# Kernel tuning notes

Hardware: AMD Instinct MI355X
Metric: run time of the kernel (lower is better)

The kernel has to match this reference:

```python
import jax, jax.numpy as jnp
import numpy as np

IMG_SIZES = [56, 28, 14, 7]


def setup_inputs() -> dict:
    key = jax.random.key(0)
    k0, k1, k2, k3, kp = jax.random.split(key, 5)
    return {
        "feat0": jax.random.normal(k0, (8, 64, 56, 56), dtype=jnp.float32),
        "feat1": jax.random.normal(k1, (8, 128, 28, 28), dtype=jnp.float32),
        "feat2": jax.random.normal(k2, (8, 256, 14, 14), dtype=jnp.float32),
        "feat3": jax.random.normal(k3, (8, 512, 7, 7), dtype=jnp.float32),
        "pts": jax.random.normal(kp, (131072, 3), dtype=jnp.float32),
        "batch": 3,
    }


def _project(feat, h, w, size):
    # feat: [C, size, size]; h, w: [N] float in [0, 223]
    x = h / (224.0 / size)
    y = w / (224.0 / size)
    x1 = jnp.floor(x).astype(jnp.int32)
    x2 = jnp.minimum(jnp.ceil(x).astype(jnp.int32), size - 1)
    y1 = jnp.floor(y).astype(jnp.int32)
    y2 = jnp.minimum(jnp.ceil(y).astype(jnp.int32), size - 1)
    # NOTE: original casts x,y to long BEFORE computing weights (truncation),
    # so weights are integer 0/1 -- reproduced faithfully.
    xl = x.astype(jnp.int32)
    yl = y.astype(jnp.int32)
    g = lambda xi, yi: feat[:, xi, yi].T  # [N, C] gather
    w11 = ((x2 - xl) * (y2 - yl)).astype(feat.dtype)[:, None]
    w12 = ((x2 - xl) * (yl - y1)).astype(feat.dtype)[:, None]
    w21 = ((xl - x1) * (y2 - yl)).astype(feat.dtype)[:, None]
    w22 = ((xl - x1) * (yl - y1)).astype(feat.dtype)[:, None]
    return w11 * g(x1, y1) + w21 * g(x2, y1) + w12 * g(x1, y2) + w22 * g(x2, y2)


def reference(feat0, feat1, feat2, feat3, pts, batch):
    h = 248.0 * (pts[:, 1] / pts[:, 2]) + 111.5
    w = 248.0 * (pts[:, 0] / (-pts[:, 2])) + 111.5
    h = jnp.clip(h, 0.0, 223.0)
    w = jnp.clip(w, 0.0, 223.0)
    feats = [feat0[batch], feat1[batch], feat2[batch], feat3[batch]]
    outs = [_project(f, h, w, s) for f, s in zip(feats, IMG_SIZES)]
    return jnp.concatenate(outs, axis=1)  # [N, 960]
```

## Files before the change

### kernel.cpp

```cpp
#include <hip/hip_runtime.h>
#include <hip/hip_bf16.h>

#define NPTS 131072
#define FT_TOTAL 376320

typedef float f32x4 __attribute__((ext_vector_type(4)));

__global__ __launch_bounds__(256) void k_indices(
    const float* __restrict__ pts,
    int4* __restrict__ idx4)
{
    int n = blockIdx.x * 256 + threadIdx.x;
    if (n >= NPTS) return;
    float px = pts[3 * n + 0];
    float py = pts[3 * n + 1];
    float pz = pts[3 * n + 2];
    float qh = __fdiv_rn(py, pz);
    float qw = __fdiv_rn(px, -pz);
    float h = __fadd_rn(__fmul_rn(248.0f, qh), 111.5f);
    float w = __fadd_rn(__fmul_rn(248.0f, qw), 111.5f);
    h = fminf(fmaxf(h, 0.0f), 223.0f);
    w = fminf(fmaxf(w, 0.0f), 223.0f);

    const float scl[4] = {0.25f, 0.125f, 0.0625f, 0.03125f};
    const int   S[4]   = {56, 28, 14, 7};
    int r[4];
#pragma unroll
    for (int s = 0; s < 4; ++s) {
        float x = h * scl[s];
        float y = w * scl[s];
        int x1 = (int)floorf(x);
        int x2 = min((int)ceilf(x), S[s] - 1);
        int y1 = (int)floorf(y);
        int y2 = min((int)ceilf(y), S[s] - 1);
        int bit = (x2 - x1) * (y2 - y1);
        r[s] = bit ? (x1 * S[s] + y1) : -1;
    }
    idx4[n] = make_int4(r[0], r[1], r[2], r[3]);
}

__global__ __launch_bounds__(256) void k_transpose(
    const float* __restrict__ f0,
    const float* __restrict__ f1,
    const float* __restrict__ f2,
    const float* __restrict__ f3,
    const int* __restrict__ batch,
    float* __restrict__ ft)
{
    int d = blockIdx.x * 256 + threadIdx.x;
    if (d >= FT_TOTAL) return;
    int b = *batch;
    const float* src;
    int local, c, p, hw;
    if (d < 200704) {
        local = d;          c = local & 63;  p = local >> 6; hw = 3136;
        src = f0 + (size_t)b * 64 * 3136;
    } else if (d < 301056) {
        local = d - 200704; c = local & 127; p = local >> 7; hw = 784;
        src = f1 + (size_t)b * 128 * 784;
    } else if (d < 351232) {
        local = d - 301056; c = local & 255; p = local >> 8; hw = 196;
        src = f2 + (size_t)b * 256 * 196;
    } else {
        local = d - 351232; c = local & 511; p = local >> 9; hw = 49;
        src = f3 + (size_t)b * 512 * 49;
    }
    ft[d] = src[c * hw + p];
}

__global__ __launch_bounds__(256) void k_gather(
    const int* __restrict__ idx,
    const float* __restrict__ ft,
    float* __restrict__ out)
{
    int gid = blockIdx.x * 256 + threadIdx.x;
    int n = gid / 240;
    int j = gid - n * 240;

    int s, C, toff, cb;
    if (j < 16)       { s = 0; C = 64;  toff = 0;      cb = j * 4; }
    else if (j < 48)  { s = 1; C = 128; toff = 200704; cb = (j - 16) * 4; }
    else if (j < 112) { s = 2; C = 256; toff = 301056; cb = (j - 48) * 4; }
    else              { s = 3; C = 512; toff = 351232; cb = (j - 112) * 4; }

    int id = idx[n * 4 + s];
    f32x4 v = (f32x4)(0.0f);
    if (id >= 0) {
        v = *(const f32x4*)(ft + toff + id * C + cb);
    }
    f32x4* dst = (f32x4*)(out + (size_t)n * 960 + j * 4);
    __builtin_nontemporal_store(v, dst);
}

extern "C" void kernel_launch(void* const* d_in, const int* in_sizes, int n_in,
                              void* d_out, int out_size, void* d_ws, size_t ws_size,
                              hipStream_t stream) {
    const float* f0  = (const float*)d_in[0];
    const float* f1  = (const float*)d_in[1];
    const float* f2  = (const float*)d_in[2];
    const float* f3  = (const float*)d_in[3];
    const float* pts = (const float*)d_in[4];
    const int* batch = (const int*)d_in[5];

    int4* idx4 = (int4*)d_ws;
    float* ft = (float*)((char*)d_ws + (size_t)NPTS * 16);
    float* out = (float*)d_out;

    k_indices<<<NPTS / 256, 256, 0, stream>>>(pts, idx4);
    k_transpose<<<(FT_TOTAL + 255) / 256, 256, 0, stream>>>(f0, f1, f2, f3, batch, ft);
    k_gather<<<122880, 256, 0, stream>>>((const int*)idx4, ft, out);
}
```

Baseline: 485.2 us.

## Fuse index computation into gather kernel with one wavefront per point

Removes the separate index kernel and its workspace round-trip. The gather kernel now maps one 64-lane wavefront to each point, computes the four projection indices inline, and has each lane write up to four float4 chunks of the 960-wide output row. This saves a launch and the index buffer traffic, and drops the per-thread divide by 240. In exchange every lane recomputes the division and projection math, and the fourth iteration leaves most lanes idle.

```diff
diff --git a/kernel.cpp b/kernel.cpp
--- a/kernel.cpp
+++ b/kernel.cpp
@@ -5,39 +5,6 @@
 #define FT_TOTAL 376320
 
 typedef float f32x4 __attribute__((ext_vector_type(4)));
-
-__global__ __launch_bounds__(256) void k_indices(
-    const float* __restrict__ pts,
-    int4* __restrict__ idx4)
-{
-    int n = blockIdx.x * 256 + threadIdx.x;
-    if (n >= NPTS) return;
-    float px = pts[3 * n + 0];
-    float py = pts[3 * n + 1];
-    float pz = pts[3 * n + 2];
-    float qh = __fdiv_rn(py, pz);
-    float qw = __fdiv_rn(px, -pz);
-    float h = __fadd_rn(__fmul_rn(248.0f, qh), 111.5f);
-    float w = __fadd_rn(__fmul_rn(248.0f, qw), 111.5f);
-    h = fminf(fmaxf(h, 0.0f), 223.0f);
-    w = fminf(fmaxf(w, 0.0f), 223.0f);
-
-    const float scl[4] = {0.25f, 0.125f, 0.0625f, 0.03125f};
-    const int   S[4]   = {56, 28, 14, 7};
-    int r[4];
-#pragma unroll
-    for (int s = 0; s < 4; ++s) {
-        float x = h * scl[s];
-        float y = w * scl[s];
-        int x1 = (int)floorf(x);
-        int x2 = min((int)ceilf(x), S[s] - 1);
-        int y1 = (int)floorf(y);
-        int y2 = min((int)ceilf(y), S[s] - 1);
-        int bit = (x2 - x1) * (y2 - y1);
-        r[s] = bit ? (x1 * S[s] + y1) : -1;
-    }
-    idx4[n] = make_int4(r[0], r[1], r[2], r[3]);
-}
 
 __global__ __launch_bounds__(256) void k_transpose(
     const float* __restrict__ f0,
@@ -69,27 +36,57 @@
 }
 
 __global__ __launch_bounds__(256) void k_gather(
-    const int* __restrict__ idx,
+    const float* __restrict__ pts,
     const float* __restrict__ ft,
     float* __restrict__ out)
 {
-    int gid = blockIdx.x * 256 + threadIdx.x;
-    int n = gid / 240;
-    int j = gid - n * 240;
+    int n = (blockIdx.x * 256 + threadIdx.x) >> 6;
+    int lane = threadIdx.x & 63;
 
-    int s, C, toff, cb;
-    if (j < 16)       { s = 0; C = 64;  toff = 0;      cb = j * 4; }
-    else if (j < 48)  { s = 1; C = 128; toff = 200704; cb = (j - 16) * 4; }
-    else if (j < 112) { s = 2; C = 256; toff = 301056; cb = (j - 48) * 4; }
-    else              { s = 3; C = 512; toff = 351232; cb = (j - 112) * 4; }
+    float px = pts[3 * n + 0];
+    float py = pts[3 * n + 1];
+    float pz = pts[3 * n + 2];
+    float qh = __fdiv_rn(py, pz);
+    float qw = __fdiv_rn(px, -pz);
+    float h = __fadd_rn(__fmul_rn(248.0f, qh), 111.5f);
+    float w = __fadd_rn(__fmul_rn(248.0f, qw), 111.5f);
+    h = fminf(fmaxf(h, 0.0f), 223.0f);
+    w = fminf(fmaxf(w, 0.0f), 223.0f);
 
-    int id = idx[n * 4 + s];
-    f32x4 v = (f32x4)(0.0f);
-    if (id >= 0) {
-        v = *(const f32x4*)(ft + toff + id * C + cb);
+    const float scl[4] = {0.25f, 0.125f, 0.0625f, 0.03125f};
+    const int   S[4]   = {56, 28, 14, 7};
+    int r[4];
+#pragma unroll
+    for (int s = 0; s < 4; ++s) {
+        float x = h * scl[s];
+        float y = w * scl[s];
+        int x1 = (int)floorf(x);
+        int x2 = min((int)ceilf(x), S[s] - 1);
+        int y1 = (int)floorf(y);
+        int y2 = min((int)ceilf(y), S[s] - 1);
+        int bit = (x2 - x1) * (y2 - y1);
+        r[s] = bit ? (x1 * S[s] + y1) : -1;
     }
-    f32x4* dst = (f32x4*)(out + (size_t)n * 960 + j * 4);
-    __builtin_nontemporal_store(v, dst);
+
+    float* rowout = out + (size_t)n * 960;
+#pragma unroll
+    for (int k = 0; k < 4; ++k) {
+        int j = 64 * k + lane;
+        if (j < 240) {
+            int s = (j >= 16) + (j >= 48) + (j >= 112);
+            int C    = 64 << s;
+            int toff = (s == 0) ? 0 : (s == 1) ? 200704 : (s == 2) ? 301056 : 351232;
+            int jb   = (s == 0) ? 0 : (s == 1) ? 16     : (s == 2) ? 48     : 112;
+            int cb   = (j - jb) * 4;
+
+            int id = r[s];
+            f32x4 v = (f32x4)(0.0f);
+            if (id >= 0) {
+                v = *(const f32x4*)(ft + toff + id * C + cb);
+            }
+            __builtin_nontemporal_store(v, (f32x4*)(rowout + j * 4));
+        }
+    }
 }
 
 extern "C" void kernel_launch(void* const* d_in, const int* in_sizes, int n_in,
@@ -102,11 +99,9 @@
     const float* pts = (const float*)d_in[4];
     const int* batch = (const int*)d_in[5];
 
-    int4* idx4 = (int4*)d_ws;
-    float* ft = (float*)((char*)d_ws + (size_t)NPTS * 16);
+    float* ft = (float*)d_ws;
     float* out = (float*)d_out;
 
-    k_indices<<<NPTS / 256, 256, 0, stream>>>(pts, idx4);
     k_transpose<<<(FT_TOTAL + 255) / 256, 256, 0, stream>>>(f0, f1, f2, f3, batch, ft);
-    k_gather<<<122880, 256, 0, stream>>>((const int*)idx4, ft, out);
+    k_gather<<<NPTS / 4, 256, 0, stream>>>(pts, ft, out);
 }
```

Result: no change. 488.3 us (+0.6%).

## Stage coarse-scale feature tables in LDS and use persistent specialized gather blocks

Applied to the files above, without the earlier changes.

Replaces the one-thread-per-float4 gather with a fixed grid of persistent blocks, each assigned a role. Scale 3 and scale 2 tables are split into channel slices that fit in 49 KB of LDS, and blocks loop over points reading from LDS. Scales 0 and 1 are still gathered from global memory in a grid-stride loop. The goal is to cut global/L2 gather traffic and per-thread index math, at the cost of lower occupancy from the large LDS footprint and possible load imbalance between block roles.

```diff
diff --git a/kernel.cpp b/kernel.cpp
--- a/kernel.cpp
+++ b/kernel.cpp
@@ -3,6 +3,15 @@
 
 #define NPTS 131072
 #define FT_TOTAL 376320
+
+#define FT1_F4 50176
+#define FT2_F4 75264
+#define FT3_F4 87808
+
+#define NB_T3 512
+#define NB_T2 128
+#define NB_T6 512
+#define GRID_GATHER (2*NB_T3 + 4*NB_T2 + NB_T6)
 
 typedef float f32x4 __attribute__((ext_vector_type(4)));
 
@@ -69,27 +78,66 @@
 }
 
 __global__ __launch_bounds__(256) void k_gather(
-    const int* __restrict__ idx,
+    const int4* __restrict__ idx,
     const float* __restrict__ ft,
     float* __restrict__ out)
 {
-    int gid = blockIdx.x * 256 + threadIdx.x;
-    int n = gid / 240;
-    int j = gid - n * 240;
+    __shared__ float lds[12544];
+    const f32x4* ft4 = (const f32x4*)ft;
+    f32x4* lds4 = (f32x4*)lds;
+    f32x4* out4 = (f32x4*)out;
+    int bid = blockIdx.x;
+    int tid = threadIdx.x;
 
-    int s, C, toff, cb;
-    if (j < 16)       { s = 0; C = 64;  toff = 0;      cb = j * 4; }
-    else if (j < 48)  { s = 1; C = 128; toff = 200704; cb = (j - 16) * 4; }
-    else if (j < 112) { s = 2; C = 256; toff = 301056; cb = (j - 48) * 4; }
-    else              { s = 3; C = 512; toff = 351232; cb = (j - 112) * 4; }
-
-    int id = idx[n * 4 + s];
-    f32x4 v = (f32x4)(0.0f);
-    if (id >= 0) {
-        v = *(const f32x4*)(ft + toff + id * C + cb);
+    if (bid < 2 * NB_T3) {
+        int s = bid / NB_T3;
+        int blk = bid - s * NB_T3;
+        for (int i = tid; i < 3136; i += 256) {
+            int r = i >> 6, c4 = i & 63;
+            lds4[i] = ft4[FT3_F4 + r * 128 + 64 * s + c4];
+        }
+        __syncthreads();
+        int wave = tid >> 6, lane = tid & 63;
+        for (int p = blk * 4 + wave; p < NPTS; p += NB_T3 * 4) {
+            int id = idx[p].w;
+            f32x4 v = (f32x4)(0.0f);
+            if (id >= 0) v = lds4[id * 64 + lane];
+            __builtin_nontemporal_store(v, &out4[p * 240 + 112 + s * 64 + lane]);
+        }
+    } else if (bid < 2 * NB_T3 + 4 * NB_T2) {
+        int rem = bid - 2 * NB_T3;
+        int s = rem / NB_T2;
+        int blk = rem - s * NB_T2;
+        for (int i = tid; i < 3136; i += 256) {
+            int r = i >> 4, c4 = i & 15;
+            lds4[i] = ft4[FT2_F4 + r * 64 + 16 * s + c4];
+        }
+        __syncthreads();
+        int wave = tid >> 6, lane = tid & 63;
+        int sub = lane >> 4, c = lane & 15;
+        for (int p0 = blk * 16 + wave * 4; p0 < NPTS; p0 += NB_T2 * 16) {
+            int p = p0 + sub;
+            int id = idx[p].z;
+            f32x4 v = (f32x4)(0.0f);
+            if (id >= 0) v = lds4[id * 16 + c];
+            __builtin_nontemporal_store(v, &out4[p * 240 + 48 + s * 16 + c]);
+        }
+    } else {
+        int blk = bid - (2 * NB_T3 + 4 * NB_T2);
+        const int TOT = NPTS * 48;
+        for (int u = blk * 256 + tid; u < TOT; u += NB_T6 * 256) {
+            int p = u / 48;
+            int c = u - p * 48;
+            int2 q = *(const int2*)&idx[p];
+            f32x4 v = (f32x4)(0.0f);
+            if (c < 16) {
+                if (q.x >= 0) v = ft4[q.x * 16 + c];
+            } else {
+                if (q.y >= 0) v = ft4[FT1_F4 + q.y * 32 + (c - 16)];
+            }
+            __builtin_nontemporal_store(v, &out4[p * 240 + c]);
+        }
     }
-    f32x4* dst = (f32x4*)(out + (size_t)n * 960 + j * 4);
-    __builtin_nontemporal_store(v, dst);
 }
 
 extern "C" void kernel_launch(void* const* d_in, const int* in_sizes, int n_in,
@@ -108,5 +156,5 @@
 
     k_indices<<<NPTS / 256, 256, 0, stream>>>(pts, idx4);
     k_transpose<<<(FT_TOTAL + 255) / 256, 256, 0, stream>>>(f0, f1, f2, f3, batch, ft);
-    k_gather<<<122880, 256, 0, stream>>>((const int*)idx4, ft, out);
+    k_gather<<<GRID_GATHER, 256, 0, stream>>>(idx4, ft, out);
 }
```

New measurement: 524.3 us. +8.0%, slower.
